# Kernel tuning notes

Hardware: AMD Instinct MI355X
Metric: run time of the kernel (lower is better)

Reference implementation:

```python
import jax, jax.numpy as jnp
import numpy as np

D = 4096          # input_dim == output_dim (square FAUST factors)
N = 1024          # batch rows of U
NNZ = 131072      # nonzeros per factor (32 per row)
K = 4             # number of sparse factors


def setup_inputs() -> dict:
    key = jax.random.key(0)
    k_u, k_b, k_v, k_r, k_c = jax.random.split(key, 5)
    U = jax.random.normal(k_u, (N, D), dtype=jnp.float32)
    bias = jax.random.normal(k_b, (D,), dtype=jnp.float32)
    # glorot-ish scaling: ~32 nnz per row -> scale by 1/sqrt(32) for stable chain
    vals = jax.random.normal(k_v, (K, NNZ), dtype=jnp.float32) * (1.0 / np.sqrt(32.0))
    rows = jax.random.randint(k_r, (K, NNZ), 0, D, dtype=jnp.int32)
    cols = jax.random.randint(k_c, (K, NNZ), 0, D, dtype=jnp.int32)
    return {"U": U, "bias": bias, "vals": vals, "rows": rows, "cols": cols}


def _spmm(rows, cols, vals, X):
    # sparse (COO) [D, D] @ dense X [D, N] -> [D, N]
    return jax.ops.segment_sum(vals[:, None] * X[cols], rows, num_segments=D)


def reference(U, bias, vals, rows, cols):
    # torch code applies sparse_matrices[-1] first, then [k-2] ... [0]
    y = U.T  # [D, N]
    for i in range(K - 1, -1, -1):
        y = _spmm(rows[i], cols[i], vals[i], y)
    return y.T + bias  # [N, D]
```

## Files before the change

kernel.cpp:

```cpp
#include <hip/hip_runtime.h>

#define D_DIM 4096
#define N_DIM 1024
#define NNZ_F 131072
#define K_F 4
#define NCHUNK 8
#define LPR 16
#define RPB 16
#define MAXE 1024
#define XS8 (N_DIM / 8)

#define T_TILES ((D_DIM / 64) * (N_DIM / 64))
#define TSTRIDE 132

__device__ __forceinline__ unsigned short f2bf(float f) {
    union { float f; unsigned int u; } v; v.f = f;
    unsigned int r = v.u + 0x7fffu + ((v.u >> 16) & 1u);
    return (unsigned short)(r >> 16);
}
__device__ __forceinline__ float bf_lo(unsigned int w) {
    return __uint_as_float(w << 16);
}
__device__ __forceinline__ float bf_hi(unsigned int w) {
    return __uint_as_float(w & 0xffff0000u);
}

__global__ __launch_bounds__(1024) void fused_t_build_k(const float* __restrict__ in,
                                                        unsigned short* __restrict__ outb,
                                                        const int* __restrict__ rows,
                                                        int* __restrict__ row_ptr_g,
                                                        int* __restrict__ cursor_g,
                                                        int* __restrict__ srow_g) {
    __shared__ int s_cnt[4 * D_DIM];
    __shared__ int s_part[1024];
    const int tid = threadIdx.x;
    const int bid = blockIdx.x;

    if (bid >= K_F) {
        const int tb = bid - K_F;
        float (*tile)[65] = (float (*)[65])s_cnt;
        const int gxi = tb & 63;
        const int gyi = tb >> 6;
        const int c0 = gxi * 64;
        const int r0 = gyi * 64;
        const int tx = tid & 63;
        const int ty = tid >> 6;
#pragma unroll
        for (int i = ty; i < 64; i += 16)
            tile[i][tx] = in[(size_t)(r0 + i) * D_DIM + c0 + tx];
        __syncthreads();
        const int px = (tid & 15) * 4;
        const int py = tid >> 4;
        ushort4 w;
        w.x = f2bf(tile[px + 0][py]);
        w.y = f2bf(tile[px + 1][py]);
        w.z = f2bf(tile[px + 2][py]);
        w.w = f2bf(tile[px + 3][py]);
        *(ushort4*)&outb[(size_t)(c0 + py) * N_DIM + r0 + px] = w;
        return;
    }

    const int f = bid;
    const int grp = (tid >> 8) & 3;
#pragma unroll
    for (int k = 0; k < 16; ++k) s_cnt[tid + k * 1024] = 0;
    __syncthreads();

    int* h = s_cnt + grp * D_DIM;
    const int4* rp4 = (const int4*)(rows + (size_t)f * NNZ_F);
#pragma unroll 4
    for (int it = 0; it < NNZ_F / 4096; ++it) {
        int4 r4 = rp4[(size_t)it * 1024 + tid];
        atomicAdd(&h[r4.x], 1);
        atomicAdd(&h[r4.y], 1);
        atomicAdd(&h[r4.z], 1);
        atomicAdd(&h[r4.w], 1);
    }
    __syncthreads();

    int c[4];
#pragma unroll
    for (int k = 0; k < 4; ++k)
        c[k] = s_cnt[tid * 4 + k] + s_cnt[D_DIM + tid * 4 + k]
             + s_cnt[2 * D_DIM + tid * 4 + k] + s_cnt[3 * D_DIM + tid * 4 + k];
    const int b = tid * 4;

    int*   rp   = row_ptr_g + (size_t)f * (D_DIM + 1);
    int*   cur  = cursor_g + (size_t)f * D_DIM;
    int*   srow = srow_g + (size_t)f * D_DIM;

    if (f == 0) {
        const int part = c[0] + c[1] + c[2] + c[3];
        s_part[tid] = part;
        __syncthreads();
        for (int off = 1; off < 1024; off <<= 1) {
            int v = (tid >= off) ? s_part[tid - off] : 0;
            __syncthreads();
            s_part[tid] += v;
            __syncthreads();
        }
        int excl = s_part[tid] - part;
#pragma unroll
        for (int k = 0; k < 4; ++k) {
            rp[b + k] = excl; cur[b + k] = excl; srow[b + k] = b + k; excl += c[k];
        }
        if (tid == 1023) rp[D_DIM] = NNZ_F;
        return;
    }

    __syncthreads();
    int* hist = s_cnt + 4096;
    int* binc = s_cnt + 4352;
    int* sA   = s_cnt + 4608;
    int* sB   = s_cnt + 4864;
    if (tid < 256) { hist[tid] = 0; binc[tid] = 0; }
    __syncthreads();
#pragma unroll
    for (int k = 0; k < 4; ++k) {
        int l = c[k] > 255 ? 255 : c[k];
        atomicAdd(&hist[l], 1);
    }
    __syncthreads();
    if (tid < 256) { int hv = hist[tid]; sA[tid] = hv; sB[tid] = hv * tid; }
    __syncthreads();
    for (int off = 1; off < 256; off <<= 1) {
        int a = 0, bb = 0;
        if (tid < 256 && tid >= off) { a = sA[tid - off]; bb = sB[tid - off]; }
        __syncthreads();
        if (tid < 256) { sA[tid] += a; sB[tid] += bb; }
        __syncthreads();
    }
#pragma unroll
    for (int k = 0; k < 4; ++k) {
        const int l = c[k] > 255 ? 255 : c[k];
        const int idx = atomicAdd(&binc[l], 1);
        const int pos    = sA[l] - hist[l] + idx;
        const int startp = sB[l] - hist[l] * l + idx * l;
        srow[pos] = b + k;
        rp[pos] = startp;
        cur[b + k] = startp;
    }
    if (tid == 1023) rp[D_DIM] = NNZ_F;
}

__global__ __launch_bounds__(1024) void scatter_all_k(const int* __restrict__ rows,
                                                      const int* __restrict__ cols,
                                                      const float* __restrict__ vals,
                                                      int* __restrict__ cursor,
                                                      int* __restrict__ csr_col,
                                                      float* __restrict__ csr_val) {
    const int f = blockIdx.x >> 7;
    const size_t j = (size_t)(blockIdx.x & 127) * 1024 + threadIdx.x;
    const size_t base = (size_t)f * NNZ_F;
    int r = rows[base + j];
    int p = atomicAdd(&cursor[(size_t)f * D_DIM + r], 1);
    csr_col[base + p] = cols[base + j];
    csr_val[base + p] = vals[base + j];
}

template <bool FINAL>
__global__ __launch_bounds__(256) void spmm_chunk_k(const int* __restrict__ row_ptr,
                                                    const int* __restrict__ sorted_rows,
                                                    const int* __restrict__ csr_col,
                                                    const float* __restrict__ csr_val,
                                                    const char* __restrict__ Xb,
                                                    uint4* __restrict__ Y,
                                                    float* __restrict__ out,
                                                    const float* __restrict__ bias) {
    __shared__ float smem[16 * TSTRIDE];
    int*   s_col  = (int*)smem;
    float* s_val  = smem + MAXE;
    int*   s_ptr  = (int*)(smem + 2 * MAXE);
    int*   s_srow = (int*)(smem + 2 * MAXE + 32);

    const int tid   = threadIdx.x;
    const int chunk = blockIdx.x & (NCHUNK - 1);
    const int rg    = blockIdx.x >> 3;
    const int r0    = rg * RPB;
    const int sub   = tid >> 4;
    const int lane  = tid & 15;
    const int slot  = chunk * LPR + lane;
    const unsigned sl16 = (unsigned)slot * 16u;

    if (tid <= RPB) s_ptr[tid] = row_ptr[r0 + tid];
    if (tid < RPB)  s_srow[tid] = sorted_rows[r0 + tid];
    __syncthreads();
    const int base  = s_ptr[0];
    const int total = s_ptr[RPB] - base;
    const int start = s_ptr[sub] - base;
    const int end_  = s_ptr[sub + 1] - base;
    const int r     = s_srow[sub];

    float acc[8];
#pragma unroll
    for (int k = 0; k < 8; ++k) acc[k] = 0.f;

    for (int cb2 = 0; cb2 < total; cb2 += MAXE) {
        int cnt = total - cb2;
        if (cnt > MAXE) cnt = MAXE;
        for (int t = tid; t < cnt; t += 256) {
            s_col[t] = csr_col[base + cb2 + t];
            s_val[t] = csr_val[base + cb2 + t];
        }
        __syncthreads();
        const int js = start > cb2 ? start : cb2;
        const int je = end_ < cb2 + cnt ? end_ : cb2 + cnt;
        int j = js;
#pragma unroll 2
        for (; j + 1 < je; j += 2) {
            const int j0 = j - cb2;
            const unsigned o0 = ((unsigned)s_col[j0] << 11) + sl16;
            const unsigned o1 = ((unsigned)s_col[j0 + 1] << 11) + sl16;
            const uint4 x0 = *(const uint4*)(Xb + o0);
            const uint4 x1 = *(const uint4*)(Xb + o1);
            const float v0 = s_val[j0];
            const float v1 = s_val[j0 + 1];
            acc[0] += v0 * bf_lo(x0.x); acc[1] += v0 * bf_hi(x0.x);
            acc[2] += v0 * bf_lo(x0.y); acc[3] += v0 * bf_hi(x0.y);
            acc[4] += v0 * bf_lo(x0.z); acc[5] += v0 * bf_hi(x0.z);
            acc[6] += v0 * bf_lo(x0.w); acc[7] += v0 * bf_hi(x0.w);
            acc[0] += v1 * bf_lo(x1.x); acc[1] += v1 * bf_hi(x1.x);
            acc[2] += v1 * bf_lo(x1.y); acc[3] += v1 * bf_hi(x1.y);
            acc[4] += v1 * bf_lo(x1.z); acc[5] += v1 * bf_hi(x1.z);
            acc[6] += v1 * bf_lo(x1.w); acc[7] += v1 * bf_hi(x1.w);
        }
        if (j < je) {
            const int j0 = j - cb2;
            const unsigned o0 = ((unsigned)s_col[j0] << 11) + sl16;
            const uint4 x0 = *(const uint4*)(Xb + o0);
            const float v0 = s_val[j0];
            acc[0] += v0 * bf_lo(x0.x); acc[1] += v0 * bf_hi(x0.x);
            acc[2] += v0 * bf_lo(x0.y); acc[3] += v0 * bf_hi(x0.y);
            acc[4] += v0 * bf_lo(x0.z); acc[5] += v0 * bf_hi(x0.z);
            acc[6] += v0 * bf_lo(x0.w); acc[7] += v0 * bf_hi(x0.w);
        }
        __syncthreads();
    }

    if (!FINAL) {
        uint4 o;
        o.x = (unsigned int)f2bf(acc[0]) | ((unsigned int)f2bf(acc[1]) << 16);
        o.y = (unsigned int)f2bf(acc[2]) | ((unsigned int)f2bf(acc[3]) << 16);
        o.z = (unsigned int)f2bf(acc[4]) | ((unsigned int)f2bf(acc[5]) << 16);
        o.w = (unsigned int)f2bf(acc[6]) | ((unsigned int)f2bf(acc[7]) << 16);
        Y[(size_t)r * XS8 + slot] = o;
    } else {
        __syncthreads();
        float* tile = smem;
        const int wbase = sub * TSTRIDE + lane * 8;
        *(float4*)&tile[wbase]     = make_float4(acc[0], acc[1], acc[2], acc[3]);
        *(float4*)&tile[wbase + 4] = make_float4(acc[4], acc[5], acc[6], acc[7]);
        __syncthreads();
        const int n0 = chunk * (N_DIM / NCHUNK);
#pragma unroll
        for (int t = tid; t < 512; t += 256) {
            const int n_loc = t >> 2;
            const int q     = t & 3;
            float4 o;
            o.x = tile[(q * 4 + 0) * TSTRIDE + n_loc];
            o.y = tile[(q * 4 + 1) * TSTRIDE + n_loc];
            o.z = tile[(q * 4 + 2) * TSTRIDE + n_loc];
            o.w = tile[(q * 4 + 3) * TSTRIDE + n_loc];
            const float4 bv = *(const float4*)&bias[r0 + q * 4];
            o.x += bv.x; o.y += bv.y; o.z += bv.z; o.w += bv.w;
            *(float4*)&out[(size_t)(n0 + n_loc) * D_DIM + r0 + q * 4] = o;
        }
    }
}

extern "C" void kernel_launch(void* const* d_in, const int* in_sizes, int n_in,
                              void* d_out, int out_size, void* d_ws, size_t ws_size,
                              hipStream_t stream) {
    const float* U    = (const float*)d_in[0];
    const float* bias = (const float*)d_in[1];
    const float* vals = (const float*)d_in[2];
    const int*   rows = (const int*)d_in[3];
    const int*   cols = (const int*)d_in[4];
    float* out = (float*)d_out;

    char* ws = (char*)d_ws;
    size_t off = 0;
    char* bufA = ws;                   off += (size_t)D_DIM * N_DIM * 2;
    char* bufB = ws + off;             off += (size_t)D_DIM * N_DIM * 2;
    int* row_ptr = (int*)(ws + off);   off += (size_t)K_F * (D_DIM + 1) * 4;
    off = (off + 15) & ~(size_t)15;
    int* cursor  = (int*)(ws + off);   off += (size_t)K_F * D_DIM * 4;
    int* srow    = (int*)(ws + off);   off += (size_t)K_F * D_DIM * 4;
    int*   csr_col = (int*)(ws + off); off += (size_t)K_F * NNZ_F * 4;
    float* csr_val = (float*)(ws + off); off += (size_t)K_F * NNZ_F * 4;

    const int grid_spmm = (D_DIM / RPB) * NCHUNK;

    fused_t_build_k<<<T_TILES + K_F, 1024, 0, stream>>>(
        U, (unsigned short*)bufA, rows, row_ptr, cursor, srow);

    scatter_all_k<<<K_F * (NNZ_F / 1024), 1024, 0, stream>>>(rows, cols, vals, cursor,
                                                             csr_col, csr_val);

    spmm_chunk_k<false><<<grid_spmm, 256, 0, stream>>>(
        row_ptr + 3 * (D_DIM + 1), srow + 3 * D_DIM,
        csr_col + 3 * (size_t)NNZ_F, csr_val + 3 * (size_t)NNZ_F,
        (const char*)bufA, (uint4*)bufB, nullptr, nullptr);
    spmm_chunk_k<false><<<grid_spmm, 256, 0, stream>>>(
        row_ptr + 2 * (D_DIM + 1), srow + 2 * D_DIM,
        csr_col + 2 * (size_t)NNZ_F, csr_val + 2 * (size_t)NNZ_F,
        (const char*)bufB, (uint4*)bufA, nullptr, nullptr);
    spmm_chunk_k<false><<<grid_spmm, 256, 0, stream>>>(
        row_ptr + 1 * (D_DIM + 1), srow + 1 * D_DIM,
        csr_col + 1 * (size_t)NNZ_F, csr_val + 1 * (size_t)NNZ_F,
        (const char*)bufA, (uint4*)bufB, nullptr, nullptr);
    spmm_chunk_k<true><<<grid_spmm, 256, 0, stream>>>(
        row_ptr + 0 * (D_DIM + 1), srow + 0 * D_DIM,
        csr_col + 0 * (size_t)NNZ_F, csr_val + 0 * (size_t)NNZ_F,
        (const char*)bufB, nullptr, out, bias);
}
```

Measured before the change: 111.2 us.

## Fuse COO-to-CSR scatter into build kernel and pack col/val pairs

Drops the separate scatter kernel. Each factor's build block now scatters its own 131072 nonzeros using per-row cursors held in shared memory instead of global atomics. Column and value are packed into a single uint2, with the column pre-shifted into a byte offset, so the SpMM staging loop does one 8-byte load per entry and skips the shift. This saves a kernel launch and global atomic traffic. The cost is that the scatter now runs on only 4 blocks, serialized inside the build kernel, which may lengthen that kernel's critical path.

```diff
diff --git a/kernel.cpp b/kernel.cpp
--- a/kernel.cpp
+++ b/kernel.cpp
@@ -28,9 +28,11 @@
 __global__ __launch_bounds__(1024) void fused_t_build_k(const float* __restrict__ in,
                                                         unsigned short* __restrict__ outb,
                                                         const int* __restrict__ rows,
+                                                        const int* __restrict__ cols,
+                                                        const float* __restrict__ vals,
                                                         int* __restrict__ row_ptr_g,
-                                                        int* __restrict__ cursor_g,
-                                                        int* __restrict__ srow_g) {
+                                                        int* __restrict__ srow_g,
+                                                        uint2* __restrict__ csr_g) {
     __shared__ int s_cnt[4 * D_DIM];
     __shared__ int s_part[1024];
     const int tid = threadIdx.x;
@@ -67,7 +69,8 @@
     __syncthreads();
 
     int* h = s_cnt + grp * D_DIM;
-    const int4* rp4 = (const int4*)(rows + (size_t)f * NNZ_F);
+    const size_t fbase = (size_t)f * NNZ_F;
+    const int4* rp4 = (const int4*)(rows + fbase);
 #pragma unroll 4
     for (int it = 0; it < NNZ_F / 4096; ++it) {
         int4 r4 = rp4[(size_t)it * 1024 + tid];
@@ -85,9 +88,10 @@
              + s_cnt[2 * D_DIM + tid * 4 + k] + s_cnt[3 * D_DIM + tid * 4 + k];
     const int b = tid * 4;
 
-    int*   rp   = row_ptr_g + (size_t)f * (D_DIM + 1);
-    int*   cur  = cursor_g + (size_t)f * D_DIM;
-    int*   srow = srow_g + (size_t)f * D_DIM;
+    int* rp   = row_ptr_g + (size_t)f * (D_DIM + 1);
+    int* srow = srow_g + (size_t)f * D_DIM;
+    int* s_cur = s_cnt + 2 * D_DIM;
+    __syncthreads();
 
     if (f == 0) {
         const int part = c[0] + c[1] + c[2] + c[3];
@@ -102,76 +106,67 @@
         int excl = s_part[tid] - part;
 #pragma unroll
         for (int k = 0; k < 4; ++k) {
-            rp[b + k] = excl; cur[b + k] = excl; srow[b + k] = b + k; excl += c[k];
-        }
-        if (tid == 1023) rp[D_DIM] = NNZ_F;
-        return;
-    }
-
-    __syncthreads();
-    int* hist = s_cnt + 4096;
-    int* binc = s_cnt + 4352;
-    int* sA   = s_cnt + 4608;
-    int* sB   = s_cnt + 4864;
-    if (tid < 256) { hist[tid] = 0; binc[tid] = 0; }
-    __syncthreads();
-#pragma unroll
-    for (int k = 0; k < 4; ++k) {
-        int l = c[k] > 255 ? 255 : c[k];
-        atomicAdd(&hist[l], 1);
-    }
-    __syncthreads();
-    if (tid < 256) { int hv = hist[tid]; sA[tid] = hv; sB[tid] = hv * tid; }
-    __syncthreads();
-    for (int off = 1; off < 256; off <<= 1) {
-        int a = 0, bb = 0;
-        if (tid < 256 && tid >= off) { a = sA[tid - off]; bb = sB[tid - off]; }
-        __syncthreads();
-        if (tid < 256) { sA[tid] += a; sB[tid] += bb; }
-        __syncthreads();
-    }
-#pragma unroll
-    for (int k = 0; k < 4; ++k) {
-        const int l = c[k] > 255 ? 255 : c[k];
-        const int idx = atomicAdd(&binc[l], 1);
-        const int pos    = sA[l] - hist[l] + idx;
-        const int startp = sB[l] - hist[l] * l + idx * l;
-        srow[pos] = b + k;
-        rp[pos] = startp;
-        cur[b + k] = startp;
+            rp[b + k] = excl; s_cur[b + k] = excl; srow[b + k] = b + k; excl += c[k];
+        }
+    } else {
+        int* hist = s_cnt + 4096;
+        int* binc = s_cnt + 4352;
+        int* sA   = s_cnt + 4608;
+        int* sB   = s_cnt + 4864;
+        if (tid < 256) { hist[tid] = 0; binc[tid] = 0; }
+        __syncthreads();
+#pragma unroll
+        for (int k = 0; k < 4; ++k) {
+            int l = c[k] > 255 ? 255 : c[k];
+            atomicAdd(&hist[l], 1);
+        }
+        __syncthreads();
+        if (tid < 256) { int hv = hist[tid]; sA[tid] = hv; sB[tid] = hv * tid; }
+        __syncthreads();
+        for (int off = 1; off < 256; off <<= 1) {
+            int a = 0, bb = 0;
+            if (tid < 256 && tid >= off) { a = sA[tid - off]; bb = sB[tid - off]; }
+            __syncthreads();
+            if (tid < 256) { sA[tid] += a; sB[tid] += bb; }
+            __syncthreads();
+        }
+#pragma unroll
+        for (int k = 0; k < 4; ++k) {
+            const int l = c[k] > 255 ? 255 : c[k];
+            const int idx = atomicAdd(&binc[l], 1);
+            const int pos    = sA[l] - hist[l] + idx;
+            const int startp = sB[l] - hist[l] * l + idx * l;
+            srow[pos] = b + k;
+            rp[pos] = startp;
+            s_cur[b + k] = startp;
+        }
     }
     if (tid == 1023) rp[D_DIM] = NNZ_F;
-}
-
-__global__ __launch_bounds__(1024) void scatter_all_k(const int* __restrict__ rows,
-                                                      const int* __restrict__ cols,
-                                                      const float* __restrict__ vals,
-                                                      int* __restrict__ cursor,
-                                                      int* __restrict__ csr_col,
-                                                      float* __restrict__ csr_val) {
-    const int f = blockIdx.x >> 7;
-    const size_t j = (size_t)(blockIdx.x & 127) * 1024 + threadIdx.x;
-    const size_t base = (size_t)f * NNZ_F;
-    int r = rows[base + j];
-    int p = atomicAdd(&cursor[(size_t)f * D_DIM + r], 1);
-    csr_col[base + p] = cols[base + j];
-    csr_val[base + p] = vals[base + j];
+    __syncthreads();
+
+    uint2* csr = csr_g + fbase;
+#pragma unroll 4
+    for (int it = 0; it < NNZ_F / 1024; ++it) {
+        const int j = it * 1024 + tid;
+        const int r = rows[fbase + j];
+        const int p = atomicAdd(&s_cur[r], 1);
+        csr[p] = make_uint2((unsigned)cols[fbase + j] << 11,
+                            __float_as_uint(vals[fbase + j]));
+    }
 }
 
 template <bool FINAL>
 __global__ __launch_bounds__(256) void spmm_chunk_k(const int* __restrict__ row_ptr,
                                                     const int* __restrict__ sorted_rows,
-                                                    const int* __restrict__ csr_col,
-                                                    const float* __restrict__ csr_val,
+                                                    const uint2* __restrict__ csr,
                                                     const char* __restrict__ Xb,
                                                     uint4* __restrict__ Y,
                                                     float* __restrict__ out,
                                                     const float* __restrict__ bias) {
     __shared__ float smem[16 * TSTRIDE];
-    int*   s_col  = (int*)smem;
-    float* s_val  = smem + MAXE;
-    int*   s_ptr  = (int*)(smem + 2 * MAXE);
-    int*   s_srow = (int*)(smem + 2 * MAXE + 32);
+    uint2* s_ent  = (uint2*)smem;
+    int*   s_ptr  = (int*)smem + 2048;
+    int*   s_srow = (int*)smem + 2072;
 
     const int tid   = threadIdx.x;
     const int chunk = blockIdx.x & (NCHUNK - 1);
@@ -198,10 +193,8 @@
     for (int cb2 = 0; cb2 < total; cb2 += MAXE) {
         int cnt = total - cb2;
         if (cnt > MAXE) cnt = MAXE;
-        for (int t = tid; t < cnt; t += 256) {
-            s_col[t] = csr_col[base + cb2 + t];
-            s_val[t] = csr_val[base + cb2 + t];
-        }
+        for (int t = tid; t < cnt; t += 256)
+            s_ent[t] = csr[base + cb2 + t];
         __syncthreads();
         const int js = start > cb2 ? start : cb2;
         const int je = end_ < cb2 + cnt ? end_ : cb2 + cnt;
@@ -209,12 +202,12 @@
 #pragma unroll 2
         for (; j + 1 < je; j += 2) {
             const int j0 = j - cb2;
-            const unsigned o0 = ((unsigned)s_col[j0] << 11) + sl16;
-            const unsigned o1 = ((unsigned)s_col[j0 + 1] << 11) + sl16;
-            const uint4 x0 = *(const uint4*)(Xb + o0);
-            const uint4 x1 = *(const uint4*)(Xb + o1);
-            const float v0 = s_val[j0];
-            const float v1 = s_val[j0 + 1];
+            const uint2 e0 = s_ent[j0];
+            const uint2 e1 = s_ent[j0 + 1];
+            const uint4 x0 = *(const uint4*)(Xb + (e0.x + sl16));
+            const uint4 x1 = *(const uint4*)(Xb + (e1.x + sl16));
+            const float v0 = __uint_as_float(e0.y);
+            const float v1 = __uint_as_float(e1.y);
             acc[0] += v0 * bf_lo(x0.x); acc[1] += v0 * bf_hi(x0.x);
             acc[2] += v0 * bf_lo(x0.y); acc[3] += v0 * bf_hi(x0.y);
             acc[4] += v0 * bf_lo(x0.z); acc[5] += v0 * bf_hi(x0.z);
@@ -226,9 +219,9 @@
         }
         if (j < je) {
             const int j0 = j - cb2;
-            const unsigned o0 = ((unsigned)s_col[j0] << 11) + sl16;
-            const uint4 x0 = *(const uint4*)(Xb + o0);
-            const float v0 = s_val[j0];
+            const uint2 e0 = s_ent[j0];
+            const uint4 x0 = *(const uint4*)(Xb + (e0.x + sl16));
+            const float v0 = __uint_as_float(e0.y);
             acc[0] += v0 * bf_lo(x0.x); acc[1] += v0 * bf_hi(x0.x);
             acc[2] += v0 * bf_lo(x0.y); acc[3] += v0 * bf_hi(x0.y);
             acc[4] += v0 * bf_lo(x0.z); acc[5] += v0 * bf_hi(x0.z);
@@ -284,33 +277,25 @@
     char* bufB = ws + off;             off += (size_t)D_DIM * N_DIM * 2;
     int* row_ptr = (int*)(ws + off);   off += (size_t)K_F * (D_DIM + 1) * 4;
     off = (off + 15) & ~(size_t)15;
-    int* cursor  = (int*)(ws + off);   off += (size_t)K_F * D_DIM * 4;
     int* srow    = (int*)(ws + off);   off += (size_t)K_F * D_DIM * 4;
-    int*   csr_col = (int*)(ws + off); off += (size_t)K_F * NNZ_F * 4;
-    float* csr_val = (float*)(ws + off); off += (size_t)K_F * NNZ_F * 4;
+    off = (off + 15) & ~(size_t)15;
+    uint2* csr   = (uint2*)(ws + off); off += (size_t)K_F * NNZ_F * 8;
 
     const int grid_spmm = (D_DIM / RPB) * NCHUNK;
 
     fused_t_build_k<<<T_TILES + K_F, 1024, 0, stream>>>(
-        U, (unsigned short*)bufA, rows, row_ptr, cursor, srow);
-
-    scatter_all_k<<<K_F * (NNZ_F / 1024), 1024, 0, stream>>>(rows, cols, vals, cursor,
-                                                             csr_col, csr_val);
+        U, (unsigned short*)bufA, rows, cols, vals, row_ptr, srow, csr);
 
     spmm_chunk_k<false><<<grid_spmm, 256, 0, stream>>>(
-        row_ptr + 3 * (D_DIM + 1), srow + 3 * D_DIM,
-        csr_col + 3 * (size_t)NNZ_F, csr_val + 3 * (size_t)NNZ_F,
+        row_ptr + 3 * (D_DIM + 1), srow + 3 * D_DIM, csr + 3 * (size_t)NNZ_F,
         (const char*)bufA, (uint4*)bufB, nullptr, nullptr);
     spmm_chunk_k<false><<<grid_spmm, 256, 0, stream>>>(
-        row_ptr + 2 * (D_DIM + 1), srow + 2 * D_DIM,
-        csr_col + 2 * (size_t)NNZ_F, csr_val + 2 * (size_t)NNZ_F,
+        row_ptr + 2 * (D_DIM + 1), srow + 2 * D_DIM, csr + 2 * (size_t)NNZ_F,
         (const char*)bufB, (uint4*)bufA, nullptr, nullptr);
     spmm_chunk_k<false><<<grid_spmm, 256, 0, stream>>>(
-        row_ptr + 1 * (D_DIM + 1), srow + 1 * D_DIM,
-        csr_col + 1 * (size_t)NNZ_F, csr_val + 1 * (size_t)NNZ_F,
+        row_ptr + 1 * (D_DIM + 1), srow + 1 * D_DIM, csr + 1 * (size_t)NNZ_F,
         (const char*)bufA, (uint4*)bufB, nullptr, nullptr);
     spmm_chunk_k<true><<<grid_spmm, 256, 0, stream>>>(
-        row_ptr + 0 * (D_DIM + 1), srow + 0 * D_DIM,
-        csr_col + 0 * (size_t)NNZ_F, csr_val + 0 * (size_t)NNZ_F,
+        row_ptr + 0 * (D_DIM + 1), srow + 0 * D_DIM, csr + 0 * (size_t)NNZ_F,
         (const char*)bufB, nullptr, out, bias);
 }
```

After: 242.5 us. +118.0%, slower.
